# Kernel tuning notes

Hardware: AMD Instinct MI355X
Metric: run time of the kernel (lower is better)

The kernel has to match this reference:

```python
import jax, jax.numpy as jnp
import numpy as np

W_GRID, H_GRID = 5, 5
N_NODES = W_GRID * H_GRID  # 25
N_NEI = 8
N_CLS = 10
BN_EPS = 1e-5


def _neighbors(i, w, h):
    """Replicates Brain.neighbors ordering exactly; pads missing slots with -1
    (the torch code pads with p1 == zeros at the END of the list)."""
    size = w * h
    n = []
    if i - w >= 0:
        n.append(i - w)
    if i % w != 0:
        n.append(i - 1)
    if (i + 1) % w != 0:
        n.append(i + 1)
    if i + w < size:
        n.append(i + w)
    if i - w - 1 >= 0 and i % w != 0:
        n.append(i - w - 1)
    if i - w + 1 >= 0 and (i + 1) % w != 0:
        n.append(i - w + 1)
    if i + w - 1 < size and i % w != 0:
        n.append(i + w - 1)
    if i + w + 1 < size and (i + 1) % w != 0:
        n.append(i + w + 1)
    while len(n) < N_NEI:
        n.append(-1)
    return n

NEI = np.array([_neighbors(i, W_GRID, H_GRID) for i in range(N_NODES)], dtype=np.int32)  # [25, 8]
NEI_CLIP = np.maximum(NEI, 0)
NEI_MASK = (NEI >= 0)


def conv_bn_relu(x, W, b, g, be, m, v):
    # Conv2d(k=3, s=1, p=1) + eval-mode BatchNorm2d + ReLU, NCHW layout
    y = jax.lax.conv_general_dilated(
        x, W, window_strides=(1, 1), padding=[(1, 1), (1, 1)],
        dimension_numbers=("NCHW", "OIHW", "NCHW"))
    y = y + b[None, :, None, None]
    scale = g / jnp.sqrt(v + BN_EPS)
    y = (y - m[None, :, None, None]) * scale[None, :, None, None] + be[None, :, None, None]
    return jax.nn.relu(y)


def maxpool3s2p1(x):
    # MaxPool2d(kernel=3, stride=2, padding=1)
    return jax.lax.reduce_window(
        x, -jnp.inf, jax.lax.max,
        window_dimensions=(1, 1, 3, 3), window_strides=(1, 1, 2, 2),
        padding=[(0, 0), (0, 0), (1, 1), (1, 1)])


def per_node_mlp(inp, Wa, ba, Wb, bb):
    # inp: [25, B, 336]; distinct Linear(336,600)-Tanh-Linear(600,10)-Softmax per node
    h = jnp.tanh(jnp.einsum("nbi,nih->nbh", inp, Wa) + ba[:, None, :])
    logits = jnp.einsum("nbh,nhc->nbc", h, Wb) + bb[:, None, :]
    return jax.nn.softmax(logits, axis=-1)  # [25, B, 10]


def setup_inputs() -> dict:
    key = jax.random.key(0)
    ks = iter(jax.random.split(key, 64))
    B, C = 8192, 3
    d = {"x": jax.random.normal(next(ks), (B, C, 20, 20), jnp.float32)}
    chans = [(C, 64), (64, 128), (128, 256), (256, 256)]
    for li, (ci, co) in enumerate(chans, start=1):
        d[f"W{li}"] = jax.random.normal(next(ks), (co, ci, 3, 3), jnp.float32) * 0.05
        d[f"b{li}"] = jax.random.normal(next(ks), (co,), jnp.float32) * 0.05
        d[f"g{li}"] = jax.random.uniform(next(ks), (co,), jnp.float32, 0.5, 1.5)
        d[f"be{li}"] = jax.random.normal(next(ks), (co,), jnp.float32) * 0.1
        d[f"m{li}"] = jax.random.normal(next(ks), (co,), jnp.float32) * 0.1
        d[f"v{li}"] = jax.random.uniform(next(ks), (co,), jnp.float32, 0.5, 1.5)
    d["Wa"] = jax.random.normal(next(ks), (N_NODES, 336, 600), jnp.float32) * 0.05
    d["ba"] = jax.random.normal(next(ks), (N_NODES, 600), jnp.float32) * 0.05
    d["Wb"] = jax.random.normal(next(ks), (N_NODES, 600, N_CLS), jnp.float32) * 0.05
    d["bb"] = jax.random.normal(next(ks), (N_NODES, N_CLS), jnp.float32) * 0.05
    return d


def reference(x, W1, b1, g1, be1, m1, v1, W2, b2, g2, be2, m2, v2,
              W3, b3, g3, be3, m3, v3, W4, b4, g4, be4, m4, v4,
              Wa, ba, Wb, bb):
    c = conv_bn_relu(x, W1, b1, g1, be1, m1, v1)
    c = maxpool3s2p1(c)                      # [B, 64, 10, 10]
    c = conv_bn_relu(c, W2, b2, g2, be2, m2, v2)
    c = maxpool3s2p1(c)                      # [B, 128, 5, 5]
    c = conv_bn_relu(c, W3, b3, g3, be3, m3, v3)
    c = conv_bn_relu(c, W4, b4, g4, be4, m4, v4)  # [B, 256, 5, 5]
    B = x.shape[0]
    feats = c.reshape(B, 256, N_NODES).transpose(2, 0, 1)  # [25, B, 256]
    # Stage 1: neighbor slots are all zeros (p1..p8 = zeros)
    zeros80 = jnp.zeros((N_NODES, B, N_NEI * N_CLS), x.dtype)
    preds = per_node_mlp(jnp.concatenate([zeros80, feats], axis=-1), Wa, ba, Wb, bb)  # [25, B, 10]
    # Stage 2: gather up to 8 neighbor predictions (ordered), pad missing with zeros
    nb = preds[jnp.asarray(NEI_CLIP)]                          # [25, 8, B, 10]
    nb = jnp.where(jnp.asarray(NEI_MASK)[:, :, None, None], nb, 0.0)
    nb = nb.transpose(0, 2, 1, 3).reshape(N_NODES, B, N_NEI * N_CLS)  # [25, B, 80]
    second = per_node_mlp(jnp.concatenate([nb, feats], axis=-1), Wa, ba, Wb, bb)  # [25, B, 10]
    mean_predictions = second.mean(axis=0)  # [B, 10]
    return mean_predictions, second
```

## Files before the change

kernel.cpp:

```cpp
#include <hip/hip_runtime.h>

typedef unsigned short u16;
typedef unsigned int u32;

typedef __attribute__((ext_vector_type(8))) __bf16 bf16x8;
typedef __attribute__((ext_vector_type(4))) float f32x4;

__device__ __forceinline__ float bf2f(u16 u) {
    u32 t = ((u32)u) << 16;
    float f;
    __builtin_memcpy(&f, &t, 4);
    return f;
}
__device__ __forceinline__ u16 f2bf(float f) {
    u32 u;
    __builtin_memcpy(&u, &f, 4);
    u32 r = (u + 0x7fffu + ((u >> 16) & 1u)) >> 16;
    return (u16)r;
}
__device__ __forceinline__ float tanh_fast(float x) {
    float xc = fminf(fmaxf(x, -15.f), 15.f);
    float e = __expf(2.f * xc);
    return (e - 1.f) * __builtin_amdgcn_rcpf(e + 1.f);
}

__device__ __forceinline__ void gld16(const u16* g, u16* l) {
    __builtin_amdgcn_global_load_lds(
        (const __attribute__((address_space(1))) u32*)(uintptr_t)g,
        (__attribute__((address_space(3))) u32*)(u32)(uintptr_t)l,
        16, 0, 0);
}



template <int EPI, int NT>
__global__ __launch_bounds__(256, 3) void gemm_bt(
    const u16* __restrict__ A, const u16* __restrict__ W, u16* __restrict__ O,
    const float* __restrict__ epiA, const float* __restrict__ epiB,
    int Kin, int N, int T, int Himg, int Wimg,
    int ldA, int ldW, int ldO,
    long long Az, long long Wz, long long Oz, int epiZ,
    int Bc, int bshift)
{
    constexpr int NJ = NT / 32;
    __shared__ __align__(16) u16 lsA[2][128 * 32];
    __shared__ __align__(16) u16 lsW[2][NT * 32];

    const int tid = threadIdx.x;
    const int z = blockIdx.z;
    A += (long long)z * Az;
    W += (long long)z * Wz;
    O += (long long)z * Oz;
    epiB += (long long)z * epiZ;

    const int m0 = blockIdx.x * 128;
    const int n0 = blockIdx.y * NT;
    const int s = m0 >> bshift;
    const int b0 = m0 & (Bc - 1);
    const int hh0 = s / Wimg, ww0 = s % Wimg;

    const int wave = tid >> 6;
    const int lane = tid & 63;
    const int mbase = (wave >> 1) * 64;
    const int nbase = (wave & 1) * (NT / 2);
    const int ln = lane & 15, qd = lane >> 4;

    const int srow = lane >> 2;
    const int sc = (((lane & 3) - ((srow >> 1) & 3)) & 3) * 8;
    const int csel = ((qd + (ln >> 1)) & 3) * 8;

    const int rowA = wave * 32 + srow;
    const int rowW = (NT == 128) ? (wave * 32 + srow) : (wave * 16 + srow);
    const int offA0 = rowA * ldA + sc;
    const int offA1 = offA0 + 16 * ldA;
    const int offW0 = rowW * ldW + sc;
    const int offW1 = offW0 + 16 * ldW;
    u16* const lA0 = &lsA[0][0] + wave * 1024;
    u16* const lW0 = (NT == 128) ? (&lsW[0][0] + wave * 1024) : (&lsW[0][0] + wave * 512);
    constexpr int LPAR_A = 128 * 32;
    constexpr int LPAR_W = NT * 32;

    auto tapvalid = [&](int t) -> bool {
        if (T != 9) return true;
        const int hh = hh0 + t / 3 - 1, ww = ww0 + t % 3 - 1;
        return hh >= 0 && hh < Himg && ww >= 0 && ww < Wimg;
    };
    auto tapA = [&](int t) -> const u16* {
        int sp = s;
        if (T == 9) sp = (hh0 + t / 3 - 1) * Wimg + (ww0 + t % 3 - 1);
        return A + (long long)(sp * Bc + b0) * ldA;
    };

    int t0 = 0;
    while (!tapvalid(t0)) ++t0;
    int nvalid = 0;
    for (int t = 0; t < T; ++t) nvalid += tapvalid(t) ? 1 : 0;
    const int KS = Kin >> 5;
    const int S = nvalid * KS;

    const u16* Ab = tapA(t0);
    const u16* Wb = W + ((long long)t0 * N + n0) * ldW;

    gld16(Ab + offA0, lA0);
    gld16(Ab + offA1, lA0 + 512);
    gld16(Wb + offW0, lW0);
    if (NT == 128) gld16(Wb + offW1, lW0 + 512);

    int ntap = t0, nkk = 0;

    f32x4 acc[4][NJ];
#pragma unroll
    for (int i = 0; i < 4; ++i)
#pragma unroll
        for (int j = 0; j < NJ; ++j)
            acc[i][j] = (f32x4){0.f, 0.f, 0.f, 0.f};

    for (int st = 0; st < S; ++st) {
        __syncthreads();
        if (st + 1 < S) {
            nkk += 32;
            if (nkk == Kin) {
                nkk = 0;
                do { ++ntap; } while (!tapvalid(ntap));
                Ab = tapA(ntap);
                Wb = W + ((long long)ntap * N + n0) * ldW;
            }
            const int pp = (st + 1) & 1;
            gld16(Ab + offA0 + nkk, lA0 + pp * LPAR_A);
            gld16(Ab + offA1 + nkk, lA0 + pp * LPAR_A + 512);
            gld16(Wb + offW0 + nkk, lW0 + pp * LPAR_W);
            if (NT == 128) gld16(Wb + offW1 + nkk, lW0 + pp * LPAR_W + 512);
        }
        const int cp = st & 1;
        bf16x8 af[4], bfr[NJ];
#pragma unroll
        for (int f = 0; f < 4; ++f)
            af[f] = *(const bf16x8*)&lsA[cp][(mbase + f * 16 + ln) * 32 + csel];
#pragma unroll
        for (int f = 0; f < NJ; ++f)
            bfr[f] = *(const bf16x8*)&lsW[cp][(nbase + f * 16 + ln) * 32 + csel];
#pragma unroll
        for (int i = 0; i < 4; ++i)
#pragma unroll
            for (int j = 0; j < NJ; ++j)
                acc[i][j] = __builtin_amdgcn_mfma_f32_16x16x32_bf16(
                    af[i], bfr[j], acc[i][j], 0, 0, 0);
    }

#pragma unroll
    for (int j = 0; j < NJ; ++j) {
        const int n = n0 + nbase + j * 16 + ln;
        const float sh = epiB[n];
        float sc2 = 1.f;
        if (EPI == 0) sc2 = epiA[n];
#pragma unroll
        for (int i = 0; i < 4; ++i) {
            const int mrow = mbase + i * 16 + qd * 4;
#pragma unroll
            for (int rr = 0; rr < 4; ++rr) {
                float v = acc[i][j][rr];
                if (EPI == 0) v = fmaxf(v * sc2 + sh, 0.f);
                else          v = tanh_fast(v + sh);
                O[(long long)(m0 + mrow + rr) * ldO + n] = f2bf(v);
            }
        }
    }
}

template <int STAGE>
__global__ __launch_bounds__(256, 2) void mlp_head(
    const u16* __restrict__ A, const u16* __restrict__ W,
    const float* __restrict__ bap, const u16* __restrict__ Wbp,
    const float* __restrict__ bbp,
    u16* __restrict__ preds, float* __restrict__ dout,
    int Kin, int Bc, int gbase)
{
    __shared__ __align__(16) u16 lsA[2][128 * 32];
    __shared__ __align__(16) u16 lsW[2][128 * 32];
    __shared__ __align__(16) u16 lsH[128 * 132];

    const int tid = threadIdx.x;
    const int z = blockIdx.z;
    A += (long long)z * Bc * Kin;
    W += (long long)z * 640 * 352;
    const float* bz = bap + z * 640;

    const int m0 = blockIdx.x * 128;
    const int wave = tid >> 6;
    const int lane = tid & 63;
    const int mbase = (wave >> 1) * 64;
    const int nbase = (wave & 1) * 64;
    const int ln = lane & 15, qd = lane >> 4;
    const int srow = lane >> 2;
    const int sc = (((lane & 3) - ((srow >> 1) & 3)) & 3) * 8;
    const int csel = ((qd + (ln >> 1)) & 3) * 8;

    const int rowS = wave * 32 + srow;
    const int offA0 = rowS * Kin + sc;
    const int offA1 = offA0 + 16 * Kin;
    const int offW0 = rowS * 352 + sc;
    const int offW1 = offW0 + 16 * 352;
    u16* const lA0 = &lsA[0][0] + wave * 1024;
    u16* const lW0 = &lsW[0][0] + wave * 1024;

    const int KS = Kin >> 5;
    const int Stot = 5 * KS;

    const u16* Ab = A + (long long)m0 * Kin;
    const u16* Wb = W;
    int pnt = 0, pnkk = 0;

    gld16(Ab + offA0, lA0);
    gld16(Ab + offA1, lA0 + 512);
    gld16(Wb + offW0, lW0);
    gld16(Wb + offW1, lW0 + 512);

    f32x4 acc[4][4];
#pragma unroll
    for (int i = 0; i < 4; ++i)
#pragma unroll
        for (int j = 0; j < 4; ++j)
            acc[i][j] = (f32x4){0.f, 0.f, 0.f, 0.f};
    f32x4 acc_lg[2];
    acc_lg[0] = (f32x4){0.f, 0.f, 0.f, 0.f};
    acc_lg[1] = (f32x4){0.f, 0.f, 0.f, 0.f};

    int g = 0;
    for (int nt = 0; nt < 5; ++nt) {
        for (int st = 0; st < KS; ++st, ++g) {
            __syncthreads();
            if (g + 1 < Stot) {
                pnkk += 32;
                if (pnkk == Kin) {
                    pnkk = 0;
                    ++pnt;
                    Wb = W + (long long)pnt * 128 * 352;
                }
                const int pp = (g + 1) & 1;
                gld16(Ab + offA0 + pnkk, lA0 + pp * (128 * 32));
                gld16(Ab + offA1 + pnkk, lA0 + pp * (128 * 32) + 512);
                gld16(Wb + offW0 + pnkk, lW0 + pp * (128 * 32));
                gld16(Wb + offW1 + pnkk, lW0 + pp * (128 * 32) + 512);
            }
            const int cp = g & 1;
            bf16x8 af[4], bfr[4];
#pragma unroll
            for (int f = 0; f < 4; ++f)
                af[f] = *(const bf16x8*)&lsA[cp][(mbase + f * 16 + ln) * 32 + csel];
#pragma unroll
            for (int f = 0; f < 4; ++f)
                bfr[f] = *(const bf16x8*)&lsW[cp][(nbase + f * 16 + ln) * 32 + csel];
#pragma unroll
            for (int i = 0; i < 4; ++i)
#pragma unroll
                for (int j = 0; j < 4; ++j)
                    acc[i][j] = __builtin_amdgcn_mfma_f32_16x16x32_bf16(
                        af[i], bfr[j], acc[i][j], 0, 0, 0);
        }

#pragma unroll
        for (int j = 0; j < 4; ++j) {
            const int hc = nbase + j * 16 + ln;
            const float sh = bz[nt * 128 + hc];
#pragma unroll
            for (int i = 0; i < 4; ++i) {
                const int br = mbase + i * 16 + qd * 4;
#pragma unroll
                for (int rr = 0; rr < 4; ++rr)
                    lsH[(br + rr) * 132 + hc] = f2bf(tanh_fast(acc[i][j][rr] + sh));
                acc[i][j] = (f32x4){0.f, 0.f, 0.f, 0.f};
            }
        }
        bf16x8 bfrg[4];
#pragma unroll
        for (int ks = 0; ks < 4; ++ks)
            bfrg[ks] = *(const bf16x8*)&Wbp[((long long)z * 16 + ln) * 640 +
                                            nt * 128 + ks * 32 + qd * 8];
        __syncthreads();

#pragma unroll
        for (int ks = 0; ks < 4; ++ks) {
#pragma unroll
            for (int i = 0; i < 2; ++i) {
                const int base = (wave * 32 + i * 16 + ln) * 132 + ks * 32 + qd * 8;
                const uint2 u0 = *(const uint2*)&lsH[base];
                const uint2 u1 = *(const uint2*)&lsH[base + 4];
                u32 w4[4] = {u0.x, u0.y, u1.x, u1.y};
                bf16x8 a8;
                __builtin_memcpy(&a8, w4, 16);
                acc_lg[i] = __builtin_amdgcn_mfma_f32_16x16x32_bf16(
                    a8, bfrg[ks], acc_lg[i], 0, 0, 0);
            }
        }
    }

    const float bias = bbp[z * 16 + ln];
#pragma unroll
    for (int i = 0; i < 2; ++i) {
#pragma unroll
        for (int rr = 0; rr < 4; ++rr) {
            const float v = acc_lg[i][rr] + bias;
            float mx = v;
#pragma unroll
            for (int mk = 1; mk < 16; mk <<= 1)
                mx = fmaxf(mx, __shfl_xor(mx, mk));
            const float e = __expf(v - mx);
            float ssum = e;
#pragma unroll
            for (int mk = 1; mk < 16; mk <<= 1)
                ssum += __shfl_xor(ssum, mk);
            const float p = e / ssum;
            const int row = m0 + wave * 32 + i * 16 + qd * 4 + rr;
            if (ln < 10) {
                if (STAGE == 1)
                    preds[((long long)z * Bc + row) * 10 + ln] = f2bf(p);
                else
                    dout[81920 + ((long long)z * 8192 + gbase + row) * 10 + ln] = p;
            }
        }
    }
}

__global__ __launch_bounds__(256) void conv1pool(
    const u16* __restrict__ xcol, const u16* __restrict__ W1t, u16* __restrict__ p1,
    const float* __restrict__ epiA, const float* __restrict__ epiB, int Bc)
{
    const int tid = threadIdx.x;
    const int wave = tid >> 6;
    const int lane = tid & 63;
    const int ln = lane & 15, qd = lane >> 4;

    const int b0 = blockIdx.x * 128;
    const int so = blockIdx.y;
    const int ho = so / 10, wo = so % 10;

    const int mbase = (wave >> 1) * 64;
    const int nbase = (wave & 1) * 32;

    bf16x8 bfr[2];
#pragma unroll
    for (int j = 0; j < 2; ++j)
        bfr[j] = *(const bf16x8*)&W1t[(nbase + j * 16 + ln) * 32 + qd * 8];

    float sc2[2], sh[2];
#pragma unroll
    for (int j = 0; j < 2; ++j) {
        const int n = nbase + j * 16 + ln;
        sc2[j] = epiA[n];
        sh[j] = epiB[n];
    }

    f32x4 best[4][2];
#pragma unroll
    for (int i = 0; i < 4; ++i)
#pragma unroll
        for (int j = 0; j < 2; ++j)
            best[i][j] = (f32x4){0.f, 0.f, 0.f, 0.f};

#pragma unroll
    for (int st = 0; st < 9; ++st) {
        int hh = 2 * ho - 1 + st / 3;
        int ww = 2 * wo - 1 + st % 3;
        hh = hh < 0 ? 0 : (hh > 19 ? 19 : hh);
        ww = ww < 0 ? 0 : (ww > 19 ? 19 : ww);
        const u16* Ab = xcol + (long long)((hh * 20 + ww) * Bc + b0) * 32;

        bf16x8 af[4];
#pragma unroll
        for (int f = 0; f < 4; ++f)
            af[f] = *(const bf16x8*)&Ab[(mbase + f * 16 + ln) * 32 + qd * 8];

#pragma unroll
        for (int i = 0; i < 4; ++i)
#pragma unroll
            for (int j = 0; j < 2; ++j) {
                f32x4 acc = (f32x4){0.f, 0.f, 0.f, 0.f};
                acc = __builtin_amdgcn_mfma_f32_16x16x32_bf16(af[i], bfr[j], acc, 0, 0, 0);
#pragma unroll
                for (int rr = 0; rr < 4; ++rr) {
                    const float v = fmaxf(acc[rr] * sc2[j] + sh[j], 0.f);
                    best[i][j][rr] = fmaxf(best[i][j][rr], v);
                }
            }
    }

#pragma unroll
    for (int j = 0; j < 2; ++j) {
        const int n = nbase + j * 16 + ln;
#pragma unroll
        for (int i = 0; i < 4; ++i) {
            const int mrow = mbase + i * 16 + qd * 4;
#pragma unroll
            for (int rr = 0; rr < 4; ++rr)
                p1[(long long)(so * Bc + b0 + mrow + rr) * 64 + n] = f2bf(best[i][j][rr]);
        }
    }
}

__global__ __launch_bounds__(256) void transpose_x(
    const float* __restrict__ x, u16* __restrict__ xt, int Bc, int bshift)
{
    const int t = blockIdx.x * 256 + threadIdx.x;
    if (t >= 400 * Bc) return;
    const int s = t >> bshift;
    const int b = t & (Bc - 1);
    const u32 c0 = f2bf(x[((long long)b * 3 + 0) * 400 + s]);
    const u32 c1 = f2bf(x[((long long)b * 3 + 1) * 400 + s]);
    const u32 c2 = f2bf(x[((long long)b * 3 + 2) * 400 + s]);
    uint2 st;
    st.x = c0 | (c1 << 16);
    st.y = c2;
    *(uint2*)(xt + ((long long)s * Bc + b) * 4) = st;
}

__global__ __launch_bounds__(256) void im2col1(
    const u16* __restrict__ xt, u16* __restrict__ xcol, int Bc, int bshift)
{
    const int t = blockIdx.x * 256 + threadIdx.x;
    if (t >= 400 * Bc) return;
    const int s = t >> bshift;
    const int b = t & (Bc - 1);
    const int hh = s / 20, ww = s % 20;

    u32 p0, q0, p1, q1, p2, q2, p3, q3, p4, q4, p5, q5, p6, q6, p7, q7, p8, q8;
#define LOADTAP(T, P, Q)                                                      \
    {                                                                         \
        const int ih = hh + (T) / 3 - 1, iw = ww + (T) % 3 - 1;               \
        P = 0u; Q = 0u;                                                       \
        if (ih >= 0 && ih < 20 && iw >= 0 && iw < 20) {                       \
            const uint2 v = *(const uint2*)(xt +                              \
                ((long long)(ih * 20 + iw) * Bc + b) * 4);                    \
            P = v.x; Q = v.y;                                                 \
        }                                                                     \
    }
    LOADTAP(0, p0, q0) LOADTAP(1, p1, q1) LOADTAP(2, p2, q2)
    LOADTAP(3, p3, q3) LOADTAP(4, p4, q4) LOADTAP(5, p5, q5)
    LOADTAP(6, p6, q6) LOADTAP(7, p7, q7) LOADTAP(8, p8, q8)
#undef LOADTAP

    u16* o = xcol + (long long)t * 32;
    uint4 w;
    w.x = p0;                w.y = q0 | (p1 << 16);
    w.z = (p1 >> 16) | (q1 << 16);
    w.w = p2;
    *(uint4*)(o + 0) = w;
    w.x = q2 | (p3 << 16);   w.y = (p3 >> 16) | (q3 << 16);
    w.z = p4;                w.w = q4 | (p5 << 16);
    *(uint4*)(o + 8) = w;
    w.x = (p5 >> 16) | (q5 << 16);
    w.y = p6;                w.z = q6 | (p7 << 16);
    w.w = (p7 >> 16) | (q7 << 16);
    *(uint4*)(o + 16) = w;
    w.x = p8;                w.y = q8;
    w.z = 0u;                w.w = 0u;
    *(uint4*)(o + 24) = w;
}

template <int CH>
__global__ __launch_bounds__(256) void pool_k(
    const u16* __restrict__ src, u16* __restrict__ dst, int Bc, int Hi, int Ho)
{
    constexpr int G = CH / 8;
    const int t = blockIdx.x * 256 + threadIdx.x;
    const int cc = t & (G - 1);
    const int b = t / G;
    if (b >= Bc) return;
    const int so = blockIdx.y;
    const int ho = so / Ho, wo = so % Ho;
    float best[8];
#pragma unroll
    for (int e = 0; e < 8; ++e) best[e] = 0.f;
    for (int ph = 0; ph < 3; ++ph) {
        const int hh = 2 * ho - 1 + ph;
        if (hh < 0 || hh >= Hi) continue;
        for (int pw = 0; pw < 3; ++pw) {
            const int ww = 2 * wo - 1 + pw;
            if (ww < 0 || ww >= Hi) continue;
            const uint4 u = *(const uint4*)(src + ((long long)(hh * Hi + ww) * Bc + b) * CH + cc * 8);
            const u32 uw[4] = {u.x, u.y, u.z, u.w};
#pragma unroll
            for (int e = 0; e < 4; ++e) {
                best[2 * e]     = fmaxf(best[2 * e],     bf2f((u16)(uw[e] & 0xffff)));
                best[2 * e + 1] = fmaxf(best[2 * e + 1], bf2f((u16)(uw[e] >> 16)));
            }
        }
    }
    u32 pk[4];
#pragma unroll
    for (int e = 0; e < 4; ++e)
        pk[e] = (u32)f2bf(best[2 * e]) | (((u32)f2bf(best[2 * e + 1])) << 16);
    uint4 st;
    st.x = pk[0]; st.y = pk[1]; st.z = pk[2]; st.w = pk[3];
    *(uint4*)(dst + ((long long)so * Bc + b) * CH + cc * 8) = st;
}

__device__ __forceinline__ void neighbors5x5(int i, int* nb) {
    const int w = 5, size = 25;
    int cnt = 0;
    if (i - w >= 0) nb[cnt++] = i - w;
    if (i % w != 0) nb[cnt++] = i - 1;
    if ((i + 1) % w != 0) nb[cnt++] = i + 1;
    if (i + w < size) nb[cnt++] = i + w;
    if (i - w - 1 >= 0 && i % w != 0) nb[cnt++] = i - w - 1;
    if (i - w + 1 >= 0 && (i + 1) % w != 0) nb[cnt++] = i - w + 1;
    if (i + w - 1 < size && i % w != 0) nb[cnt++] = i + w - 1;
    if (i + w + 1 < size && (i + 1) % w != 0) nb[cnt++] = i + w + 1;
    for (; cnt < 8; ++cnt) nb[cnt] = -1;
}

__global__ __launch_bounds__(256) void gather_nb(
    const u16* __restrict__ preds, const u16* __restrict__ feats, u16* __restrict__ A2,
    int Bc, int bshift)
{
    const int g = blockIdx.x * 256 + threadIdx.x;
    if (g >= 25 * Bc) return;
    const int n = g >> bshift;
    const int b = g & (Bc - 1);
    int nb[8];
    neighbors5x5(n, nb);
    u16* dst = A2 + (long long)g * 352;
#pragma unroll
    for (int j = 0; j < 8; ++j) {
        u32* d32 = (u32*)(dst + j * 10);
        if (nb[j] >= 0) {
            const u32* s32 = (const u32*)(preds + ((long long)nb[j] * Bc + b) * 10);
#pragma unroll
            for (int q = 0; q < 5; ++q) d32[q] = s32[q];
        } else {
#pragma unroll
            for (int q = 0; q < 5; ++q) d32[q] = 0u;
        }
    }
    const uint4* fs = (const uint4*)(feats + (long long)g * 256);
    uint4* fd = (uint4*)(dst + 80);
#pragma unroll
    for (int q = 0; q < 32; ++q) fd[q] = fs[q];
    uint4 z;
    z.x = 0u; z.y = 0u; z.z = 0u; z.w = 0u;
    *(uint4*)(dst + 336) = z;
    *(uint4*)(dst + 344) = z;
}

__global__ __launch_bounds__(256) void mean_k(float* __restrict__ dout)
{
    const int t = blockIdx.x * 256 + threadIdx.x;
    float s = 0.f;
#pragma unroll
    for (int n = 0; n < 25; ++n) s += dout[81920 + n * 81920 + t];
    dout[t] = s * 0.04f;
}

__global__ void prep_bn_all(
    const float* b1, const float* g1, const float* be1, const float* m1, const float* v1,
    const float* b2, const float* g2, const float* be2, const float* m2, const float* v2,
    const float* b3, const float* g3, const float* be3, const float* m3, const float* v3,
    const float* b4, const float* g4, const float* be4, const float* m4, const float* v4,
    float* bnA, float* bnB)
{
    const int t = blockIdx.x * 256 + threadIdx.x;
    if (t >= 704) return;
    const float *bp, *gp, *bep, *mp, *vp;
    int idx;
    if (t < 64)       { bp=b1; gp=g1; bep=be1; mp=m1; vp=v1; idx=t; }
    else if (t < 192) { bp=b2; gp=g2; bep=be2; mp=m2; vp=v2; idx=t-64; }
    else if (t < 448) { bp=b3; gp=g3; bep=be3; mp=m3; vp=v3; idx=t-192; }
    else              { bp=b4; gp=g4; bep=be4; mp=m4; vp=v4; idx=t-448; }
    const float A = gp[idx] * rsqrtf(vp[idx] + 1e-5f);
    bnA[t] = A;
    bnB[t] = (bp[idx] - mp[idx]) * A + bep[idx];
}

__global__ void prep_w1col(const float* __restrict__ W1, u16* __restrict__ W1t)
{
    const int t = blockIdx.x * 256 + threadIdx.x;
    if (t >= 64 * 32) return;
    const int n = t >> 5, k = t & 31;
    u16 v = 0;
    if (k < 27) {
        const int tap = k / 3, ci = k % 3;
        v = f2bf(W1[n * 27 + ci * 9 + tap]);
    }
    W1t[t] = v;
}

__global__ void prep_convw(const float* __restrict__ W, u16* __restrict__ Wt, int Co, int Ci)
{
    const int t = blockIdx.x * 256 + threadIdx.x;
    const int tot = 9 * Co * Ci;
    if (t >= tot) return;
    const int sh = t / (Co * Ci);
    const int rem = t % (Co * Ci);
    const int co = rem / Ci, ci = rem % Ci;
    Wt[t] = f2bf(W[(long long)(co * Ci + ci) * 9 + sh]);
}

__global__ void prep_wat(const float* __restrict__ Wa, u16* __restrict__ Wat)
{
    const int t = blockIdx.x * 256 + threadIdx.x;
    if (t >= 25 * 640 * 352) return;
    const int n = t / (640 * 352);
    const int rem = t % (640 * 352);
    const int hcol = rem / 352;
    const int k = rem % 352;
    float v = 0.f;
    if (hcol < 600 && k < 336) v = Wa[((long long)n * 336 + k) * 600 + hcol];
    Wat[t] = f2bf(v);
}

__global__ void prep_ba(const float* __restrict__ ba, float* __restrict__ bap)
{
    const int t = blockIdx.x * 256 + threadIdx.x;
    if (t >= 25 * 640) return;
    const int n = t / 640, hcol = t % 640;
    bap[t] = (hcol < 600) ? ba[n * 600 + hcol] : 0.f;
}

__global__ void prep_wbt(const float* __restrict__ Wb, const float* __restrict__ bb,
                         u16* __restrict__ Wbp, float* __restrict__ bbp)
{
    const int t = blockIdx.x * 256 + threadIdx.x;
    if (t < 25 * 16 * 640) {
        const int n = t / (16 * 640);
        const int rem = t % (16 * 640);
        const int c = rem / 640, k = rem % 640;
        u16 v = 0;
        if (c < 10 && k < 600) v = f2bf(Wb[((long long)n * 600 + k) * 10 + c]);
        Wbp[t] = v;
    }
    if (t < 25 * 16) {
        const int n = t >> 4, c = t & 15;
        bbp[t] = (c < 10) ? bb[n * 10 + c] : -1e30f;
    }
}

extern "C" void kernel_launch(void* const* d_in, const int* in_sizes, int n_in,
                              void* d_out, int out_size, void* d_ws, size_t ws_size,
                              hipStream_t stream)
{
    (void)in_sizes; (void)n_in; (void)out_size;

    const float* x  = (const float*)d_in[0];
    const float* W1 = (const float*)d_in[1];
    const float* b1 = (const float*)d_in[2];
    const float* g1 = (const float*)d_in[3];
    const float* be1= (const float*)d_in[4];
    const float* m1 = (const float*)d_in[5];
    const float* v1 = (const float*)d_in[6];
    const float* W2 = (const float*)d_in[7];
    const float* b2 = (const float*)d_in[8];
    const float* g2 = (const float*)d_in[9];
    const float* be2= (const float*)d_in[10];
    const float* m2 = (const float*)d_in[11];
    const float* v2 = (const float*)d_in[12];
    const float* W3 = (const float*)d_in[13];
    const float* b3 = (const float*)d_in[14];
    const float* g3 = (const float*)d_in[15];
    const float* be3= (const float*)d_in[16];
    const float* m3 = (const float*)d_in[17];
    const float* v3 = (const float*)d_in[18];
    const float* W4 = (const float*)d_in[19];
    const float* b4 = (const float*)d_in[20];
    const float* g4 = (const float*)d_in[21];
    const float* be4= (const float*)d_in[22];
    const float* m4 = (const float*)d_in[23];
    const float* v4 = (const float*)d_in[24];
    const float* Wa = (const float*)d_in[25];
    const float* ba = (const float*)d_in[26];
    const float* Wb = (const float*)d_in[27];
    const float* bb = (const float*)d_in[28];
    float* dout = (float*)d_out;

    auto al = [](long long v) { return (v + 255LL) & ~255LL; };
    const long long fixedB = al(4096) + al(147456) + al(589824) + al(1179648) +
                             al(11264000) + al(64000) + al(2816) + al(2816) +
                             al(512000) + al(1600);
    int Bc = 256;
    for (int cand = 8192; cand >= 256; cand >>= 1) {
        long long need = fixedB + al(44032LL * cand);
        if (need <= (long long)ws_size) { Bc = cand; break; }
    }
    const int bshift = __builtin_ctz((unsigned)Bc);
    const int C = 8192 / Bc;

    char* wsp = (char*)d_ws;
    long long off = 0;
    auto alloc = [&](long long bytes) { long long o = off; off += al(bytes); return o; };
    u16* W1t  = (u16*)(wsp + alloc(4096));
    u16* Wt2  = (u16*)(wsp + alloc(147456));
    u16* Wt3  = (u16*)(wsp + alloc(589824));
    u16* Wt4  = (u16*)(wsp + alloc(1179648));
    u16* Wat  = (u16*)(wsp + alloc(11264000));
    float* bap = (float*)(wsp + alloc(64000));
    float* bnA = (float*)(wsp + alloc(2816));
    float* bnB = (float*)(wsp + alloc(2816));
    u16* Wbp  = (u16*)(wsp + alloc(512000));
    float* bbp = (float*)(wsp + alloc(1600));
    char* ch = wsp + alloc(44032LL * Bc);
    u16* xt   = (u16*)(ch + 0LL     * Bc);
    u16* xcol = (u16*)(ch + 3200LL  * Bc);
    u16* p1   = (u16*)(ch + 28800LL * Bc);
    u16* a2   = (u16*)(ch + 0LL     * Bc);
    u16* p2   = (u16*)(ch + 25600LL * Bc);
    u16* a3   = (u16*)(ch + 0LL     * Bc);
    u16* a4   = (u16*)(ch + 12800LL * Bc);
    u16* preds= (u16*)(ch + 25600LL * Bc);
    u16* A2   = (u16*)(ch + 26112LL * Bc);

    prep_bn_all<<<dim3(3), 256, 0, stream>>>(b1,g1,be1,m1,v1, b2,g2,be2,m2,v2,
                                             b3,g3,be3,m3,v3, b4,g4,be4,m4,v4, bnA, bnB);
    prep_w1col<<<dim3(8), 256, 0, stream>>>(W1, W1t);
    prep_convw<<<dim3(288),  256, 0, stream>>>(W2, Wt2, 128, 64);
    prep_convw<<<dim3(1152), 256, 0, stream>>>(W3, Wt3, 256, 128);
    prep_convw<<<dim3(2304), 256, 0, stream>>>(W4, Wt4, 256, 256);
    prep_wat<<<dim3(22000), 256, 0, stream>>>(Wa, Wat);
    prep_ba<<<dim3(63), 256, 0, stream>>>(ba, bap);
    prep_wbt<<<dim3(1000), 256, 0, stream>>>(Wb, bb, Wbp, bbp);

    for (int c = 0; c < C; ++c) {
        const float* xc = x + (long long)c * Bc * 1200;

        transpose_x<<<dim3(400 * Bc / 256), 256, 0, stream>>>(xc, xt, Bc, bshift);
        im2col1<<<dim3(400 * Bc / 256), 256, 0, stream>>>(xt, xcol, Bc, bshift);
        conv1pool<<<dim3(Bc / 128, 100), 256, 0, stream>>>(xcol, W1t, p1, bnA, bnB, Bc);

        gemm_bt<0,128><<<dim3(100 * Bc / 128, 1), 256, 0, stream>>>(p1, Wt2, a2, bnA + 64, bnB + 64,
            64, 128, 9, 10, 10, 64, 64, 128, 0LL, 0LL, 0LL, 0, Bc, bshift);
        pool_k<128><<<dim3(Bc * 16 / 256, 25), 256, 0, stream>>>(a2, p2, Bc, 10, 5);

        gemm_bt<0,128><<<dim3(25 * Bc / 128, 2), 256, 0, stream>>>(p2, Wt3, a3, bnA + 192, bnB + 192,
            128, 256, 9, 5, 5, 128, 128, 256, 0LL, 0LL, 0LL, 0, Bc, bshift);
        gemm_bt<0,128><<<dim3(25 * Bc / 128, 2), 256, 0, stream>>>(a3, Wt4, a4, bnA + 448, bnB + 448,
            256, 256, 9, 5, 5, 256, 256, 256, 0LL, 0LL, 0LL, 0, Bc, bshift);

        mlp_head<1><<<dim3(Bc / 128, 1, 25), 256, 0, stream>>>(
            a4, Wat + 80, bap, Wbp, bbp, preds, nullptr, 256, Bc, 0);

        gather_nb<<<dim3(25 * Bc / 256, 1), 256, 0, stream>>>(preds, a4, A2, Bc, bshift);
        mlp_head<2><<<dim3(Bc / 128, 1, 25), 256, 0, stream>>>(
            A2, Wat, bap, Wbp, bbp, nullptr, dout, 352, Bc, c * Bc);
    }

    mean_k<<<dim3(320), 256, 0, stream>>>(dout);
}
```

Measured before the change: 1.435 ms.

## Remap conv GEMM block order so interior spatial positions dispatch first

For 3x3 convolutions, the linear block index is remapped so that tiles for interior pixel positions are scheduled first, then edges, then corners. When there are two N tiles, the two column blocks of the same M tile are interleaved in groups of eight. This is meant to put heavy full-tap tiles at the front and the lighter border tiles, which skip padded taps, at the end, reducing tail imbalance and improving L2 reuse of weights and activations. The cost is some extra integer arithmetic per block, and the remap only applies when the per-position batch tile count is a multiple of eight.

```diff
diff --git a/kernel.cpp b/kernel.cpp
--- a/kernel.cpp
+++ b/kernel.cpp
@@ -53,8 +53,47 @@
     O += (long long)z * Oz;
     epiB += (long long)z * epiZ;
 
-    const int m0 = blockIdx.x * 128;
-    const int n0 = blockIdx.y * NT;
+    int m0, n0;
+    {
+        const int bps = Bc >> 7;
+        if (T == 9 && (bps & 7) == 0) {
+            const int d = blockIdx.x + gridDim.x * blockIdx.y;
+            int pairid, nidx;
+            if (gridDim.y == 2) {
+                nidx = (d >> 3) & 1;
+                pairid = ((d >> 4) << 3) | (d & 7);
+            } else {
+                pairid = d;
+                nidx = 0;
+            }
+            const int rank = pairid >> (bshift - 7);
+            const int bidx = pairid & (bps - 1);
+            const int Hm2 = Himg - 2, Wm2 = Wimg - 2;
+            const int Ni = Hm2 * Wm2;
+            const int Ne = 2 * Wm2 + 2 * Hm2;
+            int hh, ww;
+            if (rank < Ni) {
+                hh = 1 + rank / Wm2;
+                ww = 1 + rank % Wm2;
+            } else if (rank < Ni + Ne) {
+                const int e = rank - Ni;
+                if (e < Wm2)                 { hh = 0;                     ww = 1 + e; }
+                else if (e < 2 * Wm2)        { hh = Himg - 1;              ww = 1 + e - Wm2; }
+                else if (e < 2 * Wm2 + Hm2)  { hh = 1 + e - 2 * Wm2;       ww = 0; }
+                else                         { hh = 1 + e - 2 * Wm2 - Hm2; ww = Wimg - 1; }
+            } else {
+                const int c2 = rank - Ni - Ne;
+                hh = (c2 & 2) ? (Himg - 1) : 0;
+                ww = (c2 & 1) ? (Wimg - 1) : 0;
+            }
+            m0 = ((hh * Wimg + ww) * bps + bidx) * 128;
+            n0 = nidx * NT;
+        } else {
+            m0 = blockIdx.x * 128;
+            n0 = blockIdx.y * NT;
+        }
+    }
+
     const int s = m0 >> bshift;
     const int b0 = m0 & (Bc - 1);
     const int hh0 = s / Wimg, ww0 = s % Wimg;
```

Measured after the change: 1.378 ms. 4.0% less time.
